# Optimization experiments

Measured on AMD Instinct MI355X. Metric: run time of the kernel, lower is better.

Reference implementation:

```python
import jax, jax.numpy as jnp
import numpy as np

N_NODES = 20000
N_EDGES = 320000
IN_DIM = 128
HID = 64
LATENT = 32
NUM_GRAPHS = 64
NEG_SLOPE = 0.2
BN_EPS = 1e-5


def setup_inputs() -> dict:
    key = jax.random.key(0)
    ks = jax.random.split(key, 24)
    def glorot(k, shape):
        fan_in, fan_out = shape[0], shape[-1]
        lim = (6.0 / (fan_in + fan_out)) ** 0.5
        return jax.random.uniform(k, shape, jnp.float32, -lim, lim)
    inp = {
        "x": jax.random.normal(ks[0], (N_NODES, IN_DIM), jnp.float32),
        "edge_index": jax.random.randint(ks[1], (2, N_EDGES), 0, N_NODES, jnp.int64),
        "batch": jnp.sort(jax.random.randint(ks[2], (N_NODES,), 0, NUM_GRAPHS, jnp.int64)),
        # layer 0: in=128 -> out=64, heads=4
        "Wl0": glorot(ks[3], (IN_DIM, 4 * HID)),
        "Wr0": glorot(ks[4], (IN_DIM, 4 * HID)),
        "att0": glorot(ks[5], (4, HID)),
        "b0": jnp.zeros((4 * HID,), jnp.float32),
        # layer 1: in=256 -> out=64, heads=4
        "Wl1": glorot(ks[6], (4 * HID, 4 * HID)),
        "Wr1": glorot(ks[7], (4 * HID, 4 * HID)),
        "att1": glorot(ks[8], (4, HID)),
        "b1": jnp.zeros((4 * HID,), jnp.float32),
        # layer 2: in=256 -> out=64, heads=1
        "Wl2": glorot(ks[9], (4 * HID, HID)),
        "Wr2": glorot(ks[10], (4 * HID, HID)),
        "att2": glorot(ks[11], (1, HID)),
        "b2": jnp.zeros((HID,), jnp.float32),
        # BatchNorm1d(hidden_dim) in eval mode (running stats)
        "bn_gamma": jax.random.uniform(ks[12], (HID,), jnp.float32, 0.5, 1.5),
        "bn_beta": jax.random.normal(ks[13], (HID,), jnp.float32) * 0.1,
        "bn_mean": jax.random.normal(ks[14], (HID,), jnp.float32) * 0.1,
        "bn_var": jax.random.uniform(ks[15], (HID,), jnp.float32, 0.5, 1.5),
        # fc: hidden -> latent
        "fc_w": glorot(ks[16], (HID, LATENT)),
        "fc_b": jnp.zeros((LATENT,), jnp.float32),
    }
    return inp


def gatv2_layer(h, src, dst, Wl, Wr, att, bias):
    # PyG GATv2Conv (concat=True, negative_slope=0.2, self loops already in src/dst)
    N = h.shape[0]
    H, C = att.shape
    xl = (h @ Wl).reshape(N, H, C)  # source transform
    xr = (h @ Wr).reshape(N, H, C)  # target transform
    e = jax.nn.leaky_relu(xl[src] + xr[dst], NEG_SLOPE)   # [E,H,C]
    logits = jnp.einsum("ehc,hc->eh", e, att)             # [E,H]
    # softmax over incoming edges per destination node
    m = jax.ops.segment_max(logits, dst, num_segments=N)  # [N,H]
    ex = jnp.exp(logits - m[dst])
    denom = jax.ops.segment_sum(ex, dst, num_segments=N)
    alpha = ex / denom[dst]                               # [E,H]
    out = jax.ops.segment_sum(alpha[:, :, None] * xl[src], dst, num_segments=N)
    return out.reshape(N, H * C) + bias


def reference(x, edge_index, batch, Wl0, Wr0, att0, b0, Wl1, Wr1, att1, b1,
              Wl2, Wr2, att2, b2, bn_gamma, bn_beta, bn_mean, bn_var, fc_w, fc_b):
    N = x.shape[0]
    loop = jnp.arange(N, dtype=edge_index.dtype)
    src = jnp.concatenate([edge_index[0], loop])  # add self loops (PyG default)
    dst = jnp.concatenate([edge_index[1], loop])
    h = gatv2_layer(x, src, dst, Wl0, Wr0, att0, b0)   # dropout: eval mode -> identity
    h = gatv2_layer(h, src, dst, Wl1, Wr1, att1, b1)
    h = gatv2_layer(h, src, dst, Wl2, Wr2, att2, b2)   # [N, HID]
    pooled = jax.ops.segment_sum(h, batch, num_segments=NUM_GRAPHS)  # global_add_pool
    bn = (pooled - bn_mean) * jax.lax.rsqrt(bn_var + BN_EPS) * bn_gamma + bn_beta
    return bn @ fc_w + fc_b  # [NUM_GRAPHS, LATENT]
```

## Files before the change

### kernel.cpp

```cpp
#include <hip/hip_runtime.h>
#include <math.h>

#define N_NODES 20000
#define E_ORIG  320000
#define E_TOT   340000
#define NUM_GRAPHS 64
#define SLOTS 96

typedef __attribute__((ext_vector_type(8))) short bf16x8;
typedef __attribute__((ext_vector_type(4))) float f32x4;

__device__ __forceinline__ ushort f2bf(float x) {
  unsigned u = __float_as_uint(x);
  return (ushort)((u + 0x7fffu + ((u >> 16) & 1u)) >> 16);
}
__device__ __forceinline__ float4 ld_bf16x4(const ushort* p) {
  ushort4 u = *(const ushort4*)p;
  float4 f;
  f.x = __uint_as_float((unsigned)u.x << 16);
  f.y = __uint_as_float((unsigned)u.y << 16);
  f.z = __uint_as_float((unsigned)u.z << 16);
  f.w = __uint_as_float((unsigned)u.w << 16);
  return f;
}
__device__ __forceinline__ void gl_lds16(const void* g, void* l) {
  __builtin_amdgcn_global_load_lds(
      (const __attribute__((address_space(1))) unsigned*)(uintptr_t)g,
      (__attribute__((address_space(3))) unsigned*)(uintptr_t)l, 16, 0, 0);
}

__global__ __launch_bounds__(256) void prep(
    const float* __restrict__ x,
    const float* __restrict__ Wl0, const float* __restrict__ Wr0,
    const float* __restrict__ Wl1, const float* __restrict__ Wr1,
    const float* __restrict__ Wl2, const float* __restrict__ Wr2,
    ushort* __restrict__ x16, ushort* __restrict__ Bt0,
    ushort* __restrict__ Bt1, ushort* __restrict__ Bt2,
    int* __restrict__ cursor)
{
  const int Z0 = 640000;
  const int Z1 = Z0 + 65536;
  const int Z2 = Z1 + 131072;
  const int Z3 = Z2 + 32768;
  const int Z4 = Z3 + N_NODES / 4;
  int t = blockIdx.x * 256 + threadIdx.x;
  if (t < Z0) {
    int i = t << 2;
    float4 v = *(const float4*)&x[i];
    ushort4 o; o.x = f2bf(v.x); o.y = f2bf(v.y); o.z = f2bf(v.z); o.w = f2bf(v.w);
    *(ushort4*)&x16[i] = o;
  } else if (t < Z1) {
    int idx = t - Z0; int n = idx >> 7, k = idx & 127;
    float v = (n < 256) ? Wl0[k * 256 + n] : Wr0[k * 256 + (n - 256)];
    Bt0[idx] = f2bf(v);
  } else if (t < Z2) {
    int idx = t - Z1; int n = idx >> 8, k = idx & 255;
    float v = (n < 256) ? Wl1[k * 256 + n] : Wr1[k * 256 + (n - 256)];
    Bt1[idx] = f2bf(v);
  } else if (t < Z3) {
    int idx = t - Z2; int n = idx >> 8, k = idx & 255;
    float v = (n < 64) ? Wl2[k * 64 + n] : Wr2[k * 64 + (n - 64)];
    Bt2[idx] = f2bf(v);
  } else if (t < Z4) {
    int4 z = {0, 0, 0, 0};
    *(int4*)&cursor[(t - Z3) << 2] = z;
  }
}

__device__ __forceinline__ void gemm_body(
    const ushort* __restrict__ A, const ushort* __restrict__ Bt,
    ushort* __restrict__ C, int M, int K, int N, int bid, int tid, char* smem)
{
  ushort* As = (ushort*)smem;
  ushort* Bs = As + 8192;

  const int mtiles = (M + 127) >> 7;
  const int xcd = bid & 7;
  const int i = bid >> 3;
  const int n0 = (i / 20) << 7;
  const int m = xcd + ((i % 20) << 3);
  if (m >= mtiles) return;
  const int m0 = m << 7;

  const int lane = tid & 63;
  const int w = tid >> 6;
  const int wm = (w >> 1) << 6;
  const int wn = (w & 1) << 6;
  const int quad = lane >> 4;
  const int l15 = lane & 15;

  f32x4 acc[4][4] = {};

  for (int k0 = 0; k0 < K; k0 += 64) {
    #pragma unroll
    for (int r = 0; r < 4; r++) {
      int c = (r << 8) + tid;
      int row = c >> 3;
      int col = (c & 7) << 3;
      int ga = m0 + row; if (ga >= M) ga = M - 1;
      gl_lds16(A  + (size_t)ga * K + k0 + col, (char*)As + c * 16);
      gl_lds16(Bt + (size_t)(n0 + row) * K + k0 + col, (char*)Bs + c * 16);
    }
    __syncthreads();
    #pragma unroll
    for (int ks = 0; ks < 2; ks++) {
      bf16x8 af[4], bfr[4];
      #pragma unroll
      for (int ii = 0; ii < 4; ii++)
        af[ii]  = *(const bf16x8*)&As[(wm + (ii << 4) + l15) * 64 + (ks << 5) + (quad << 3)];
      #pragma unroll
      for (int j = 0; j < 4; j++)
        bfr[j] = *(const bf16x8*)&Bs[(wn + (j << 4) + l15) * 64 + (ks << 5) + (quad << 3)];
      #pragma unroll
      for (int ii = 0; ii < 4; ii++)
        #pragma unroll
        for (int j = 0; j < 4; j++)
          acc[ii][j] = __builtin_amdgcn_mfma_f32_16x16x32_bf16(
              af[ii], bfr[j], acc[ii][j], 0, 0, 0);
    }
    __syncthreads();
  }

  ushort* Cs = (ushort*)smem + w * 4608;
  #pragma unroll
  for (int ii = 0; ii < 4; ii++)
    #pragma unroll
    for (int j = 0; j < 4; j++)
      #pragma unroll
      for (int r = 0; r < 4; r++)
        Cs[((ii << 4) + (quad << 2) + r) * 72 + (j << 4) + l15] = f2bf(acc[ii][j][r]);
  #pragma unroll
  for (int it = 0; it < 8; it++) {
    int row = (it << 3) + (lane >> 3);
    int cc = lane & 7;
    bf16x8 v = *(const bf16x8*)&Cs[row * 72 + (cc << 3)];
    int grow = m0 + wm + row;
    if (grow < M)
      *(bf16x8*)&C[(size_t)grow * N + n0 + wn + (cc << 3)] = v;
  }
}

__global__ __launch_bounds__(256) void mfma_gemm_bf16(
    const ushort* __restrict__ A, const ushort* __restrict__ Bt,
    ushort* __restrict__ C, int M, int K, int N)
{
  __shared__ char smem[36864];
  gemm_body(A, Bt, C, M, K, N, blockIdx.x, threadIdx.x, smem);
}

#define FILLB 1329
__global__ __launch_bounds__(256) void gemm0_fill(
    const ushort* __restrict__ x16, const ushort* __restrict__ Bt0,
    ushort* __restrict__ Cbig,
    const int* __restrict__ esrc, const int* __restrict__ edst,
    int* __restrict__ cursor, int* __restrict__ csr_src)
{
  __shared__ char smem[36864];
  const int bid = blockIdx.x;
  if (bid < FILLB) {
    int e = bid * 256 + threadIdx.x;
    if (e >= E_TOT) return;
    int src, dst;
    if (e < E_ORIG) { src = esrc[e]; dst = edst[e]; }
    else            { src = dst = e - E_ORIG; }
    int pos = atomicAdd(&cursor[dst], 1);
    if (pos < SLOTS) csr_src[(size_t)dst * SLOTS + pos] = src;
    return;
  }
  gemm_body(x16, Bt0, Cbig, N_NODES, 128, 512, bid - FILLB, threadIdx.x, smem);
}

__device__ __forceinline__ void h4_term(
    float4 xlv, const float4& xrv, const float4& attv, float& v)
{
  float4 a;
  a.x = xlv.x + xrv.x; a.y = xlv.y + xrv.y;
  a.z = xlv.z + xrv.z; a.w = xlv.w + xrv.w;
  a.x = fmaxf(a.x, 0.2f * a.x); a.y = fmaxf(a.y, 0.2f * a.y);
  a.z = fmaxf(a.z, 0.2f * a.z); a.w = fmaxf(a.w, 0.2f * a.w);
  v = a.x * attv.x + a.y * attv.y + a.z * attv.z + a.w * attv.w;
}

__device__ __forceinline__ void h4_edge(
    const float4& xv, const float4& xrv, const float4& attv,
    float4& acc, float& lsum)
{
  float v;
  h4_term(xv, xrv, attv, v);
  v += __shfl_xor(v, 1);
  v += __shfl_xor(v, 2);
  v += __shfl_xor(v, 4);
  v += __shfl_xor(v, 8);
  float w = __expf(v);
  lsum += w;
  acc.x += w * xv.x; acc.y += w * xv.y;
  acc.z += w * xv.z; acc.w += w * xv.w;
}

__global__ __launch_bounds__(256) void gat_gather_h4(
    const ushort* __restrict__ Cin, const float* __restrict__ att,
    const float* __restrict__ bias, const int* __restrict__ cnt,
    const int* __restrict__ csr_src, ushort* __restrict__ hout)
{
  const int n = blockIdx.x * 4 + (threadIdx.x >> 6);
  const int lane = threadIdx.x & 63;
  const int c4 = lane << 2;
  const float4 xrv  = ld_bf16x4(Cin + (size_t)n * 512 + 256 + c4);
  const float4 attv = *(const float4*)&att[c4];
  const int beg = n * SLOTS;
  int deg = cnt[n]; if (deg > SLOTS) deg = SLOTS;
  const int end = beg + deg;
  float4 acc = make_float4(0.f, 0.f, 0.f, 0.f);
  float lsum = 0.f;
  int p = beg;
  for (; p + 7 < end; p += 8) {
    int s0 = csr_src[p],     s1 = csr_src[p + 1];
    int s2 = csr_src[p + 2], s3 = csr_src[p + 3];
    int s4 = csr_src[p + 4], s5 = csr_src[p + 5];
    int s6 = csr_src[p + 6], s7 = csr_src[p + 7];
    float4 x0 = ld_bf16x4(Cin + (size_t)s0 * 512 + c4);
    float4 x1 = ld_bf16x4(Cin + (size_t)s1 * 512 + c4);
    float4 x2 = ld_bf16x4(Cin + (size_t)s2 * 512 + c4);
    float4 x3 = ld_bf16x4(Cin + (size_t)s3 * 512 + c4);
    float4 x4 = ld_bf16x4(Cin + (size_t)s4 * 512 + c4);
    float4 x5 = ld_bf16x4(Cin + (size_t)s5 * 512 + c4);
    float4 x6 = ld_bf16x4(Cin + (size_t)s6 * 512 + c4);
    float4 x7 = ld_bf16x4(Cin + (size_t)s7 * 512 + c4);
    h4_edge(x0, xrv, attv, acc, lsum);
    h4_edge(x1, xrv, attv, acc, lsum);
    h4_edge(x2, xrv, attv, acc, lsum);
    h4_edge(x3, xrv, attv, acc, lsum);
    h4_edge(x4, xrv, attv, acc, lsum);
    h4_edge(x5, xrv, attv, acc, lsum);
    h4_edge(x6, xrv, attv, acc, lsum);
    h4_edge(x7, xrv, attv, acc, lsum);
  }
  for (; p + 3 < end; p += 4) {
    int s0 = csr_src[p],     s1 = csr_src[p + 1];
    int s2 = csr_src[p + 2], s3 = csr_src[p + 3];
    float4 x0 = ld_bf16x4(Cin + (size_t)s0 * 512 + c4);
    float4 x1 = ld_bf16x4(Cin + (size_t)s1 * 512 + c4);
    float4 x2 = ld_bf16x4(Cin + (size_t)s2 * 512 + c4);
    float4 x3 = ld_bf16x4(Cin + (size_t)s3 * 512 + c4);
    h4_edge(x0, xrv, attv, acc, lsum);
    h4_edge(x1, xrv, attv, acc, lsum);
    h4_edge(x2, xrv, attv, acc, lsum);
    h4_edge(x3, xrv, attv, acc, lsum);
  }
  for (; p < end; p++) {
    int s0 = csr_src[p];
    float4 x0 = ld_bf16x4(Cin + (size_t)s0 * 512 + c4);
    h4_edge(x0, xrv, attv, acc, lsum);
  }
  const float4 bv = *(const float4*)&bias[c4];
  float inv = 1.f / lsum;
  ushort4 o;
  o.x = f2bf(acc.x * inv + bv.x); o.y = f2bf(acc.y * inv + bv.y);
  o.z = f2bf(acc.z * inv + bv.z); o.w = f2bf(acc.w * inv + bv.w);
  *(ushort4*)&hout[(size_t)n * 256 + c4] = o;
}

__global__ __launch_bounds__(256) void gat_gather_h1(
    const ushort* __restrict__ Cin, const float* __restrict__ att,
    const float* __restrict__ bias, const int* __restrict__ cnt,
    const int* __restrict__ csr_src, float* __restrict__ h3)
{
  const int n = blockIdx.x * 4 + (threadIdx.x >> 6);
  const int lane = threadIdx.x & 63;
  const int g = lane >> 4, c4 = (lane & 15) << 2;
  const float4 xrv  = ld_bf16x4(Cin + (size_t)n * 128 + 64 + c4);
  const float4 attv = *(const float4*)&att[c4];
  const int beg = n * SLOTS;
  int deg = cnt[n]; if (deg > SLOTS) deg = SLOTS;
  const int end = beg + deg;
  float4 acc = make_float4(0.f, 0.f, 0.f, 0.f);
  float lsum = 0.f;
  int p = beg + g;
  for (; p + 4 < end; p += 8) {
    int s0 = csr_src[p], s1 = csr_src[p + 4];
    float4 x0 = ld_bf16x4(Cin + (size_t)s0 * 128 + c4);
    float4 x1 = ld_bf16x4(Cin + (size_t)s1 * 128 + c4);
    h4_edge(x0, xrv, attv, acc, lsum);
    h4_edge(x1, xrv, attv, acc, lsum);
  }
  if (p < end) {
    int s0 = csr_src[p];
    float4 x0 = ld_bf16x4(Cin + (size_t)s0 * 128 + c4);
    h4_edge(x0, xrv, attv, acc, lsum);
  }
  #pragma unroll
  for (int off = 16; off <= 32; off <<= 1) {
    lsum  += __shfl_xor(lsum, off);
    acc.x += __shfl_xor(acc.x, off); acc.y += __shfl_xor(acc.y, off);
    acc.z += __shfl_xor(acc.z, off); acc.w += __shfl_xor(acc.w, off);
  }
  if (g == 0) {
    const float4 bv = *(const float4*)&bias[c4];
    float inv = 1.f / lsum;
    float4 o;
    o.x = acc.x * inv + bv.x; o.y = acc.y * inv + bv.y;
    o.z = acc.z * inv + bv.z; o.w = acc.w * inv + bv.w;
    *(float4*)&h3[(size_t)n * 64 + c4] = o;
  }
}

__global__ __launch_bounds__(256) void pool_bn_fc(
    const float* __restrict__ h3, const int* __restrict__ batch,
    const float* __restrict__ gamma, const float* __restrict__ beta,
    const float* __restrict__ mean, const float* __restrict__ var,
    const float* __restrict__ fcw, const float* __restrict__ fcb,
    float* __restrict__ out)
{
  __shared__ float red[256];
  __shared__ float s[64];
  const int g = blockIdx.x;
  const int t = threadIdx.x;
  const int c = t & 63, r = t >> 6;
  int lo = 0, hi = N_NODES;
  while (lo < hi) { int mid = (lo + hi) >> 1; if (batch[mid] < g) lo = mid + 1; else hi = mid; }
  int s0 = lo;
  hi = N_NODES;
  while (lo < hi) { int mid = (lo + hi) >> 1; if (batch[mid] < g + 1) lo = mid + 1; else hi = mid; }
  int e0 = lo;
  float a = 0.f;
  for (int n = s0 + r; n < e0; n += 4) a += h3[(size_t)n * 64 + c];
  red[t] = a;
  __syncthreads();
  if (r == 0) {
    float p = red[c] + red[c + 64] + red[c + 128] + red[c + 192];
    s[c] = (p - mean[c]) * rsqrtf(var[c] + 1e-5f) * gamma[c] + beta[c];
  }
  __syncthreads();
  if (t < 32) {
    float acc = fcb[t];
    #pragma unroll
    for (int k = 0; k < 64; k++) acc += s[k] * fcw[k * 32 + t];
    out[g * 32 + t] = acc;
  }
}

extern "C" void kernel_launch(void* const* d_in, const int* in_sizes, int n_in,
                              void* d_out, int out_size, void* d_ws, size_t ws_size,
                              hipStream_t stream) {
  const float* x    = (const float*)d_in[0];
  const int*   ei   = (const int*)d_in[1];
  const int*   batch= (const int*)d_in[2];
  const float* Wl0  = (const float*)d_in[3];
  const float* Wr0  = (const float*)d_in[4];
  const float* att0 = (const float*)d_in[5];
  const float* b0   = (const float*)d_in[6];
  const float* Wl1  = (const float*)d_in[7];
  const float* Wr1  = (const float*)d_in[8];
  const float* att1 = (const float*)d_in[9];
  const float* b1   = (const float*)d_in[10];
  const float* Wl2  = (const float*)d_in[11];
  const float* Wr2  = (const float*)d_in[12];
  const float* att2 = (const float*)d_in[13];
  const float* b2   = (const float*)d_in[14];
  const float* bng  = (const float*)d_in[15];
  const float* bnb  = (const float*)d_in[16];
  const float* bnm  = (const float*)d_in[17];
  const float* bnv  = (const float*)d_in[18];
  const float* fcw  = (const float*)d_in[19];
  const float* fcb  = (const float*)d_in[20];
  float* out = (float*)d_out;

  const int* esrc = ei;
  const int* edst = ei + E_ORIG;

  char* w = (char*)d_ws;
  ushort* x16  = (ushort*)w;                 w += (size_t)N_NODES * 128 * 2;
  ushort* Cbig = (ushort*)w;                 w += (size_t)N_NODES * 512 * 2;
  ushort* h16  = (ushort*)w;                 w += (size_t)N_NODES * 256 * 2;
  ushort* C2   = (ushort*)w;                 w += (size_t)N_NODES * 128 * 2;
  float*  h3   = (float*)w;                  w += (size_t)N_NODES * 64 * 4;
  ushort* Bt0  = (ushort*)w;                 w += (size_t)512 * 128 * 2;
  ushort* Bt1  = (ushort*)w;                 w += (size_t)512 * 256 * 2;
  ushort* Bt2  = (ushort*)w;                 w += (size_t)128 * 256 * 2;
  int* cursor  = (int*)w;                    w += (size_t)N_NODES * 4;
  int* csr_src = (int*)w;

  dim3 blk(256);

  prep<<<dim3(3416), blk, 0, stream>>>(
      x, Wl0, Wr0, Wl1, Wr1, Wl2, Wr2, x16, Bt0, Bt1, Bt2, cursor);

  gemm0_fill<<<dim3(FILLB + 160 * 4), blk, 0, stream>>>(
      x16, Bt0, Cbig, esrc, edst, cursor, csr_src);

  gat_gather_h4<<<dim3(N_NODES / 4), blk, 0, stream>>>(
      Cbig, att0, b0, cursor, csr_src, h16);

  mfma_gemm_bf16<<<dim3(160 * 4), blk, 0, stream>>>(h16, Bt1, Cbig, N_NODES, 256, 512);
  gat_gather_h4<<<dim3(N_NODES / 4), blk, 0, stream>>>(
      Cbig, att1, b1, cursor, csr_src, h16);

  mfma_gemm_bf16<<<dim3(160 * 1), blk, 0, stream>>>(h16, Bt2, C2, N_NODES, 256, 128);
  gat_gather_h1<<<dim3(N_NODES / 4), blk, 0, stream>>>(
      C2, att2, b2, cursor, csr_src, h3);

  pool_bn_fc<<<dim3(NUM_GRAPHS), blk, 0, stream>>>(
      h3, batch, bng, bnb, bnm, bnv, fcw, fcb, out);
}
```

Before: 261.1 us.

## Fuse all stages into one persistent cooperative kernel with grid syncs

Replaces the eight separate launches (prep, fill plus GEMM0, three gathers, two GEMMs, pool) with one cooperative persistent kernel. Grid-stride loops cover each stage, and a grid.sync separates dependent phases. The aim is to remove per-launch overhead and inter-kernel gaps. In exchange it caps resident blocks per CU through the occupancy query and launch bounds, adds seven grid-wide barriers, and shares one 36 KB shared-memory buffer across phases, which may cost occupancy in the gather phases.

```diff
diff --git a/kernel.cpp b/kernel.cpp
--- a/kernel.cpp
+++ b/kernel.cpp
@@ -1,11 +1,24 @@
 #include <hip/hip_runtime.h>
+#include <hip/hip_cooperative_groups.h>
 #include <math.h>
+
+namespace cg = cooperative_groups;
 
 #define N_NODES 20000
 #define E_ORIG  320000
 #define E_TOT   340000
 #define NUM_GRAPHS 64
 #define SLOTS 96
+#define FILLB 1329
+#define G0B   640
+#define G1B   640
+#define G2B   160
+
+#define PZ0 640000
+#define PZ1 (PZ0 + 65536)
+#define PZ2 (PZ1 + 131072)
+#define PZ3 (PZ2 + 32768)
+#define PZ4 (PZ3 + N_NODES / 4)
 
 typedef __attribute__((ext_vector_type(8))) short bf16x8;
 typedef __attribute__((ext_vector_type(4))) float f32x4;
@@ -29,43 +42,15 @@
       (__attribute__((address_space(3))) unsigned*)(uintptr_t)l, 16, 0, 0);
 }
 
-__global__ __launch_bounds__(256) void prep(
-    const float* __restrict__ x,
-    const float* __restrict__ Wl0, const float* __restrict__ Wr0,
-    const float* __restrict__ Wl1, const float* __restrict__ Wr1,
-    const float* __restrict__ Wl2, const float* __restrict__ Wr2,
-    ushort* __restrict__ x16, ushort* __restrict__ Bt0,
-    ushort* __restrict__ Bt1, ushort* __restrict__ Bt2,
-    int* __restrict__ cursor)
-{
-  const int Z0 = 640000;
-  const int Z1 = Z0 + 65536;
-  const int Z2 = Z1 + 131072;
-  const int Z3 = Z2 + 32768;
-  const int Z4 = Z3 + N_NODES / 4;
-  int t = blockIdx.x * 256 + threadIdx.x;
-  if (t < Z0) {
-    int i = t << 2;
-    float4 v = *(const float4*)&x[i];
-    ushort4 o; o.x = f2bf(v.x); o.y = f2bf(v.y); o.z = f2bf(v.z); o.w = f2bf(v.w);
-    *(ushort4*)&x16[i] = o;
-  } else if (t < Z1) {
-    int idx = t - Z0; int n = idx >> 7, k = idx & 127;
-    float v = (n < 256) ? Wl0[k * 256 + n] : Wr0[k * 256 + (n - 256)];
-    Bt0[idx] = f2bf(v);
-  } else if (t < Z2) {
-    int idx = t - Z1; int n = idx >> 8, k = idx & 255;
-    float v = (n < 256) ? Wl1[k * 256 + n] : Wr1[k * 256 + (n - 256)];
-    Bt1[idx] = f2bf(v);
-  } else if (t < Z3) {
-    int idx = t - Z2; int n = idx >> 8, k = idx & 255;
-    float v = (n < 64) ? Wl2[k * 64 + n] : Wr2[k * 64 + (n - 64)];
-    Bt2[idx] = f2bf(v);
-  } else if (t < Z4) {
-    int4 z = {0, 0, 0, 0};
-    *(int4*)&cursor[(t - Z3) << 2] = z;
-  }
-}
+struct Params {
+  const float* x; const int* esrc; const int* edst; const int* batch;
+  const float *Wl0, *Wr0, *Wl1, *Wr1, *Wl2, *Wr2;
+  const float *att0, *b0, *att1, *b1, *att2, *b2;
+  const float *bng, *bnb, *bnm, *bnv, *fcw, *fcb;
+  float* out;
+  ushort *x16, *Cbig, *h16, *C2; float* h3;
+  ushort *Bt0, *Bt1, *Bt2; int* cursor; int* csr;
+};
 
 __device__ __forceinline__ void gemm_body(
     const ushort* __restrict__ A, const ushort* __restrict__ Bt,
@@ -140,53 +125,16 @@
   }
 }
 
-__global__ __launch_bounds__(256) void mfma_gemm_bf16(
-    const ushort* __restrict__ A, const ushort* __restrict__ Bt,
-    ushort* __restrict__ C, int M, int K, int N)
-{
-  __shared__ char smem[36864];
-  gemm_body(A, Bt, C, M, K, N, blockIdx.x, threadIdx.x, smem);
-}
-
-#define FILLB 1329
-__global__ __launch_bounds__(256) void gemm0_fill(
-    const ushort* __restrict__ x16, const ushort* __restrict__ Bt0,
-    ushort* __restrict__ Cbig,
-    const int* __restrict__ esrc, const int* __restrict__ edst,
-    int* __restrict__ cursor, int* __restrict__ csr_src)
-{
-  __shared__ char smem[36864];
-  const int bid = blockIdx.x;
-  if (bid < FILLB) {
-    int e = bid * 256 + threadIdx.x;
-    if (e >= E_TOT) return;
-    int src, dst;
-    if (e < E_ORIG) { src = esrc[e]; dst = edst[e]; }
-    else            { src = dst = e - E_ORIG; }
-    int pos = atomicAdd(&cursor[dst], 1);
-    if (pos < SLOTS) csr_src[(size_t)dst * SLOTS + pos] = src;
-    return;
-  }
-  gemm_body(x16, Bt0, Cbig, N_NODES, 128, 512, bid - FILLB, threadIdx.x, smem);
-}
-
-__device__ __forceinline__ void h4_term(
-    float4 xlv, const float4& xrv, const float4& attv, float& v)
-{
-  float4 a;
-  a.x = xlv.x + xrv.x; a.y = xlv.y + xrv.y;
-  a.z = xlv.z + xrv.z; a.w = xlv.w + xrv.w;
-  a.x = fmaxf(a.x, 0.2f * a.x); a.y = fmaxf(a.y, 0.2f * a.y);
-  a.z = fmaxf(a.z, 0.2f * a.z); a.w = fmaxf(a.w, 0.2f * a.w);
-  v = a.x * attv.x + a.y * attv.y + a.z * attv.z + a.w * attv.w;
-}
-
 __device__ __forceinline__ void h4_edge(
     const float4& xv, const float4& xrv, const float4& attv,
     float4& acc, float& lsum)
 {
-  float v;
-  h4_term(xv, xrv, attv, v);
+  float4 a;
+  a.x = xv.x + xrv.x; a.y = xv.y + xrv.y;
+  a.z = xv.z + xrv.z; a.w = xv.w + xrv.w;
+  a.x = fmaxf(a.x, 0.2f * a.x); a.y = fmaxf(a.y, 0.2f * a.y);
+  a.z = fmaxf(a.z, 0.2f * a.z); a.w = fmaxf(a.w, 0.2f * a.w);
+  float v = a.x * attv.x + a.y * attv.y + a.z * attv.z + a.w * attv.w;
   v += __shfl_xor(v, 1);
   v += __shfl_xor(v, 2);
   v += __shfl_xor(v, 4);
@@ -197,13 +145,11 @@
   acc.z += w * xv.z; acc.w += w * xv.w;
 }
 
-__global__ __launch_bounds__(256) void gat_gather_h4(
+__device__ __forceinline__ void gat_h4_node(
     const ushort* __restrict__ Cin, const float* __restrict__ att,
     const float* __restrict__ bias, const int* __restrict__ cnt,
-    const int* __restrict__ csr_src, ushort* __restrict__ hout)
-{
-  const int n = blockIdx.x * 4 + (threadIdx.x >> 6);
-  const int lane = threadIdx.x & 63;
+    const int* __restrict__ csr, ushort* __restrict__ hout, int n, int lane)
+{
   const int c4 = lane << 2;
   const float4 xrv  = ld_bf16x4(Cin + (size_t)n * 512 + 256 + c4);
   const float4 attv = *(const float4*)&att[c4];
@@ -214,10 +160,10 @@
   float lsum = 0.f;
   int p = beg;
   for (; p + 7 < end; p += 8) {
-    int s0 = csr_src[p],     s1 = csr_src[p + 1];
-    int s2 = csr_src[p + 2], s3 = csr_src[p + 3];
-    int s4 = csr_src[p + 4], s5 = csr_src[p + 5];
-    int s6 = csr_src[p + 6], s7 = csr_src[p + 7];
+    int s0 = csr[p],     s1 = csr[p + 1];
+    int s2 = csr[p + 2], s3 = csr[p + 3];
+    int s4 = csr[p + 4], s5 = csr[p + 5];
+    int s6 = csr[p + 6], s7 = csr[p + 7];
     float4 x0 = ld_bf16x4(Cin + (size_t)s0 * 512 + c4);
     float4 x1 = ld_bf16x4(Cin + (size_t)s1 * 512 + c4);
     float4 x2 = ld_bf16x4(Cin + (size_t)s2 * 512 + c4);
@@ -236,8 +182,8 @@
     h4_edge(x7, xrv, attv, acc, lsum);
   }
   for (; p + 3 < end; p += 4) {
-    int s0 = csr_src[p],     s1 = csr_src[p + 1];
-    int s2 = csr_src[p + 2], s3 = csr_src[p + 3];
+    int s0 = csr[p],     s1 = csr[p + 1];
+    int s2 = csr[p + 2], s3 = csr[p + 3];
     float4 x0 = ld_bf16x4(Cin + (size_t)s0 * 512 + c4);
     float4 x1 = ld_bf16x4(Cin + (size_t)s1 * 512 + c4);
     float4 x2 = ld_bf16x4(Cin + (size_t)s2 * 512 + c4);
@@ -248,7 +194,7 @@
     h4_edge(x3, xrv, attv, acc, lsum);
   }
   for (; p < end; p++) {
-    int s0 = csr_src[p];
+    int s0 = csr[p];
     float4 x0 = ld_bf16x4(Cin + (size_t)s0 * 512 + c4);
     h4_edge(x0, xrv, attv, acc, lsum);
   }
@@ -260,13 +206,11 @@
   *(ushort4*)&hout[(size_t)n * 256 + c4] = o;
 }
 
-__global__ __launch_bounds__(256) void gat_gather_h1(
+__device__ __forceinline__ void gat_h1_node(
     const ushort* __restrict__ Cin, const float* __restrict__ att,
     const float* __restrict__ bias, const int* __restrict__ cnt,
-    const int* __restrict__ csr_src, float* __restrict__ h3)
-{
-  const int n = blockIdx.x * 4 + (threadIdx.x >> 6);
-  const int lane = threadIdx.x & 63;
+    const int* __restrict__ csr, float* __restrict__ h3, int n, int lane)
+{
   const int g = lane >> 4, c4 = (lane & 15) << 2;
   const float4 xrv  = ld_bf16x4(Cin + (size_t)n * 128 + 64 + c4);
   const float4 attv = *(const float4*)&att[c4];
@@ -277,14 +221,14 @@
   float lsum = 0.f;
   int p = beg + g;
   for (; p + 4 < end; p += 8) {
-    int s0 = csr_src[p], s1 = csr_src[p + 4];
+    int s0 = csr[p], s1 = csr[p + 4];
     float4 x0 = ld_bf16x4(Cin + (size_t)s0 * 128 + c4);
     float4 x1 = ld_bf16x4(Cin + (size_t)s1 * 128 + c4);
     h4_edge(x0, xrv, attv, acc, lsum);
     h4_edge(x1, xrv, attv, acc, lsum);
   }
   if (p < end) {
-    int s0 = csr_src[p];
+    int s0 = csr[p];
     float4 x0 = ld_bf16x4(Cin + (size_t)s0 * 128 + c4);
     h4_edge(x0, xrv, attv, acc, lsum);
   }
@@ -304,101 +248,156 @@
   }
 }
 
-__global__ __launch_bounds__(256) void pool_bn_fc(
-    const float* __restrict__ h3, const int* __restrict__ batch,
-    const float* __restrict__ gamma, const float* __restrict__ beta,
-    const float* __restrict__ mean, const float* __restrict__ var,
-    const float* __restrict__ fcw, const float* __restrict__ fcb,
-    float* __restrict__ out)
-{
-  __shared__ float red[256];
-  __shared__ float s[64];
-  const int g = blockIdx.x;
-  const int t = threadIdx.x;
+__device__ __forceinline__ void pool_body(const Params& p, int g, int t, float* sm)
+{
+  float* red = sm;
+  float* s   = sm + 256;
   const int c = t & 63, r = t >> 6;
   int lo = 0, hi = N_NODES;
-  while (lo < hi) { int mid = (lo + hi) >> 1; if (batch[mid] < g) lo = mid + 1; else hi = mid; }
+  while (lo < hi) { int mid = (lo + hi) >> 1; if (p.batch[mid] < g) lo = mid + 1; else hi = mid; }
   int s0 = lo;
   hi = N_NODES;
-  while (lo < hi) { int mid = (lo + hi) >> 1; if (batch[mid] < g + 1) lo = mid + 1; else hi = mid; }
+  while (lo < hi) { int mid = (lo + hi) >> 1; if (p.batch[mid] < g + 1) lo = mid + 1; else hi = mid; }
   int e0 = lo;
   float a = 0.f;
-  for (int n = s0 + r; n < e0; n += 4) a += h3[(size_t)n * 64 + c];
+  for (int n = s0 + r; n < e0; n += 4) a += p.h3[(size_t)n * 64 + c];
   red[t] = a;
   __syncthreads();
   if (r == 0) {
-    float p = red[c] + red[c + 64] + red[c + 128] + red[c + 192];
-    s[c] = (p - mean[c]) * rsqrtf(var[c] + 1e-5f) * gamma[c] + beta[c];
+    float q = red[c] + red[c + 64] + red[c + 128] + red[c + 192];
+    s[c] = (q - p.bnm[c]) * rsqrtf(p.bnv[c] + 1e-5f) * p.bng[c] + p.bnb[c];
   }
   __syncthreads();
   if (t < 32) {
-    float acc = fcb[t];
+    float acc = p.fcb[t];
     #pragma unroll
-    for (int k = 0; k < 64; k++) acc += s[k] * fcw[k * 32 + t];
-    out[g * 32 + t] = acc;
-  }
+    for (int k = 0; k < 64; k++) acc += s[k] * p.fcw[k * 32 + t];
+    p.out[g * 32 + t] = acc;
+  }
+  __syncthreads();
+}
+
+__global__ __launch_bounds__(256, 3) void fused_all(Params p)
+{
+  __shared__ char smem[36864];
+  const int bid = blockIdx.x, tid = threadIdx.x;
+  const int NB = gridDim.x;
+  const int lane = tid & 63, wv = tid >> 6;
+  cg::grid_group grid = cg::this_grid();
+
+  for (int t = bid * 256 + tid; t < PZ4; t += NB * 256) {
+    if (t < PZ0) {
+      int i = t << 2;
+      float4 v = *(const float4*)&p.x[i];
+      ushort4 o; o.x = f2bf(v.x); o.y = f2bf(v.y); o.z = f2bf(v.z); o.w = f2bf(v.w);
+      *(ushort4*)&p.x16[i] = o;
+    } else if (t < PZ1) {
+      int idx = t - PZ0; int n = idx >> 7, k = idx & 127;
+      float v = (n < 256) ? p.Wl0[k * 256 + n] : p.Wr0[k * 256 + (n - 256)];
+      p.Bt0[idx] = f2bf(v);
+    } else if (t < PZ2) {
+      int idx = t - PZ1; int n = idx >> 8, k = idx & 255;
+      float v = (n < 256) ? p.Wl1[k * 256 + n] : p.Wr1[k * 256 + (n - 256)];
+      p.Bt1[idx] = f2bf(v);
+    } else if (t < PZ3) {
+      int idx = t - PZ2; int n = idx >> 8, k = idx & 255;
+      float v = (n < 64) ? p.Wl2[k * 64 + n] : p.Wr2[k * 64 + (n - 64)];
+      p.Bt2[idx] = f2bf(v);
+    } else {
+      int4 z = {0, 0, 0, 0};
+      *(int4*)&p.cursor[(t - PZ3) << 2] = z;
+    }
+  }
+  grid.sync();
+
+  for (int r = bid; r < FILLB + G0B; r += NB) {
+    if (r < FILLB) {
+      int e = r * 256 + tid;
+      if (e < E_TOT) {
+        int src, dst;
+        if (e < E_ORIG) { src = p.esrc[e]; dst = p.edst[e]; }
+        else            { src = dst = e - E_ORIG; }
+        int pos = atomicAdd(&p.cursor[dst], 1);
+        if (pos < SLOTS) p.csr[(size_t)dst * SLOTS + pos] = src;
+      }
+    } else {
+      gemm_body(p.x16, p.Bt0, p.Cbig, N_NODES, 128, 512, r - FILLB, tid, smem);
+    }
+  }
+  grid.sync();
+
+  for (int b = bid; b < N_NODES / 4; b += NB)
+    gat_h4_node(p.Cbig, p.att0, p.b0, p.cursor, p.csr, p.h16, b * 4 + wv, lane);
+  grid.sync();
+
+  for (int r = bid; r < G1B; r += NB)
+    gemm_body(p.h16, p.Bt1, p.Cbig, N_NODES, 256, 512, r, tid, smem);
+  grid.sync();
+
+  for (int b = bid; b < N_NODES / 4; b += NB)
+    gat_h4_node(p.Cbig, p.att1, p.b1, p.cursor, p.csr, p.h16, b * 4 + wv, lane);
+  grid.sync();
+
+  for (int r = bid; r < G2B; r += NB)
+    gemm_body(p.h16, p.Bt2, p.C2, N_NODES, 256, 128, r, tid, smem);
+  grid.sync();
+
+  for (int b = bid; b < N_NODES / 4; b += NB)
+    gat_h1_node(p.C2, p.att2, p.b2, p.cursor, p.csr, p.h3, b * 4 + wv, lane);
+  grid.sync();
+
+  for (int g = bid; g < NUM_GRAPHS; g += NB)
+    pool_body(p, g, tid, (float*)smem);
 }
 
 extern "C" void kernel_launch(void* const* d_in, const int* in_sizes, int n_in,
                               void* d_out, int out_size, void* d_ws, size_t ws_size,
                               hipStream_t stream) {
-  const float* x    = (const float*)d_in[0];
-  const int*   ei   = (const int*)d_in[1];
-  const int*   batch= (const int*)d_in[2];
-  const float* Wl0  = (const float*)d_in[3];
-  const float* Wr0  = (const float*)d_in[4];
-  const float* att0 = (const float*)d_in[5];
-  const float* b0   = (const float*)d_in[6];
-  const float* Wl1  = (const float*)d_in[7];
-  const float* Wr1  = (const float*)d_in[8];
-  const float* att1 = (const float*)d_in[9];
-  const float* b1   = (const float*)d_in[10];
-  const float* Wl2  = (const float*)d_in[11];
-  const float* Wr2  = (const float*)d_in[12];
-  const float* att2 = (const float*)d_in[13];
-  const float* b2   = (const float*)d_in[14];
-  const float* bng  = (const float*)d_in[15];
-  const float* bnb  = (const float*)d_in[16];
-  const float* bnm  = (const float*)d_in[17];
-  const float* bnv  = (const float*)d_in[18];
-  const float* fcw  = (const float*)d_in[19];
-  const float* fcb  = (const float*)d_in[20];
-  float* out = (float*)d_out;
-
-  const int* esrc = ei;
-  const int* edst = ei + E_ORIG;
+  const int* ei = (const int*)d_in[1];
+
+  Params p;
+  p.x    = (const float*)d_in[0];
+  p.esrc = ei;
+  p.edst = ei + E_ORIG;
+  p.batch= (const int*)d_in[2];
+  p.Wl0  = (const float*)d_in[3];
+  p.Wr0  = (const float*)d_in[4];
+  p.att0 = (const float*)d_in[5];
+  p.b0   = (const float*)d_in[6];
+  p.Wl1  = (const float*)d_in[7];
+  p.Wr1  = (const float*)d_in[8];
+  p.att1 = (const float*)d_in[9];
+  p.b1   = (const float*)d_in[10];
+  p.Wl2  = (const float*)d_in[11];
+  p.Wr2  = (const float*)d_in[12];
+  p.att2 = (const float*)d_in[13];
+  p.b2   = (const float*)d_in[14];
+  p.bng  = (const float*)d_in[15];
+  p.bnb  = (const float*)d_in[16];
+  p.bnm  = (const float*)d_in[17];
+  p.bnv  = (const float*)d_in[18];
+  p.fcw  = (const float*)d_in[19];
+  p.fcb  = (const float*)d_in[20];
+  p.out  = (float*)d_out;
 
   char* w = (char*)d_ws;
-  ushort* x16  = (ushort*)w;                 w += (size_t)N_NODES * 128 * 2;
-  ushort* Cbig = (ushort*)w;                 w += (size_t)N_NODES * 512 * 2;
-  ushort* h16  = (ushort*)w;                 w += (size_t)N_NODES * 256 * 2;
-  ushort* C2   = (ushort*)w;                 w += (size_t)N_NODES * 128 * 2;
-  float*  h3   = (float*)w;                  w += (size_t)N_NODES * 64 * 4;
-  ushort* Bt0  = (ushort*)w;                 w += (size_t)512 * 128 * 2;
-  ushort* Bt1  = (ushort*)w;                 w += (size_t)512 * 256 * 2;
-  ushort* Bt2  = (ushort*)w;                 w += (size_t)128 * 256 * 2;
-  int* cursor  = (int*)w;                    w += (size_t)N_NODES * 4;
-  int* csr_src = (int*)w;
-
-  dim3 blk(256);
-
-  prep<<<dim3(3416), blk, 0, stream>>>(
-      x, Wl0, Wr0, Wl1, Wr1, Wl2, Wr2, x16, Bt0, Bt1, Bt2, cursor);
-
-  gemm0_fill<<<dim3(FILLB + 160 * 4), blk, 0, stream>>>(
-      x16, Bt0, Cbig, esrc, edst, cursor, csr_src);
-
-  gat_gather_h4<<<dim3(N_NODES / 4), blk, 0, stream>>>(
-      Cbig, att0, b0, cursor, csr_src, h16);
-
-  mfma_gemm_bf16<<<dim3(160 * 4), blk, 0, stream>>>(h16, Bt1, Cbig, N_NODES, 256, 512);
-  gat_gather_h4<<<dim3(N_NODES / 4), blk, 0, stream>>>(
-      Cbig, att1, b1, cursor, csr_src, h16);
-
-  mfma_gemm_bf16<<<dim3(160 * 1), blk, 0, stream>>>(h16, Bt2, C2, N_NODES, 256, 128);
-  gat_gather_h1<<<dim3(N_NODES / 4), blk, 0, stream>>>(
-      C2, att2, b2, cursor, csr_src, h3);
-
-  pool_bn_fc<<<dim3(NUM_GRAPHS), blk, 0, stream>>>(
-      h3, batch, bng, bnb, bnm, bnv, fcw, fcb, out);
-}
+  p.x16  = (ushort*)w;                 w += (size_t)N_NODES * 128 * 2;
+  p.Cbig = (ushort*)w;                 w += (size_t)N_NODES * 512 * 2;
+  p.h16  = (ushort*)w;                 w += (size_t)N_NODES * 256 * 2;
+  p.C2   = (ushort*)w;                 w += (size_t)N_NODES * 128 * 2;
+  p.h3   = (float*)w;                  w += (size_t)N_NODES * 64 * 4;
+  p.Bt0  = (ushort*)w;                 w += (size_t)512 * 128 * 2;
+  p.Bt1  = (ushort*)w;                 w += (size_t)512 * 256 * 2;
+  p.Bt2  = (ushort*)w;                 w += (size_t)128 * 256 * 2;
+  p.cursor = (int*)w;                  w += (size_t)N_NODES * 4;
+  p.csr  = (int*)w;
+
+  int nb = 0;
+  hipOccupancyMaxActiveBlocksPerMultiprocessor(&nb, fused_all, 256, 0);
+  if (nb < 1) nb = 1;
+  if (nb > 4) nb = 4;
+  int grid = nb * 256;
+
+  void* args[] = { (void*)&p };
+  hipLaunchCooperativeKernel(fused_all, dim3(grid), dim3(256), args, 0, stream);
+}
```

Measured after the change: 656.3 us. +151.4%, slower.

## Split XL/XR into separate buffers, handle self-loops inline, shrink CSR slots

Applied to the files above, without the earlier changes.

The GEMM epilogue now writes the source and target projections into two separate contiguous arrays instead of one interleaved 512-wide row, so the gather reads a denser 256-wide XL array with better cache locality. Self-loop edges are no longer inserted through atomics into the CSR; each gather processes the node's own XL row directly. CSR slots shrink from 96 to 64 per node, which reduces the memory footprint but drops edges for any node whose in-degree exceeds 64.

```diff
diff --git a/kernel.cpp b/kernel.cpp
--- a/kernel.cpp
+++ b/kernel.cpp
@@ -3,9 +3,9 @@
 
 #define N_NODES 20000
 #define E_ORIG  320000
-#define E_TOT   340000
 #define NUM_GRAPHS 64
-#define SLOTS 96
+#define SLOTS 64
+#define FILLB 1250
 
 typedef __attribute__((ext_vector_type(8))) short bf16x8;
 typedef __attribute__((ext_vector_type(4))) float f32x4;
@@ -69,7 +69,8 @@
 
 __device__ __forceinline__ void gemm_body(
     const ushort* __restrict__ A, const ushort* __restrict__ Bt,
-    ushort* __restrict__ C, int M, int K, int N, int bid, int tid, char* smem)
+    ushort* __restrict__ XL, ushort* __restrict__ XR,
+    int M, int K, int N, int bid, int tid, char* smem)
 {
   ushort* As = (ushort*)smem;
   ushort* Bs = As + 8192;
@@ -129,6 +130,9 @@
       #pragma unroll
       for (int r = 0; r < 4; r++)
         Cs[((ii << 4) + (quad << 2) + r) * 72 + (j << 4) + l15] = f2bf(acc[ii][j][r]);
+  const int Nh = N >> 1;
+  const int colbase = n0 + wn;
+  ushort* Cc = (colbase < Nh) ? (XL + colbase) : (XR + (colbase - Nh));
   #pragma unroll
   for (int it = 0; it < 8; it++) {
     int row = (it << 3) + (lane >> 3);
@@ -136,22 +140,21 @@
     bf16x8 v = *(const bf16x8*)&Cs[row * 72 + (cc << 3)];
     int grow = m0 + wm + row;
     if (grow < M)
-      *(bf16x8*)&C[(size_t)grow * N + n0 + wn + (cc << 3)] = v;
+      *(bf16x8*)&Cc[(size_t)grow * Nh + (cc << 3)] = v;
   }
 }
 
 __global__ __launch_bounds__(256) void mfma_gemm_bf16(
     const ushort* __restrict__ A, const ushort* __restrict__ Bt,
-    ushort* __restrict__ C, int M, int K, int N)
+    ushort* __restrict__ XL, ushort* __restrict__ XR, int M, int K, int N)
 {
   __shared__ char smem[36864];
-  gemm_body(A, Bt, C, M, K, N, blockIdx.x, threadIdx.x, smem);
-}
-
-#define FILLB 1329
+  gemm_body(A, Bt, XL, XR, M, K, N, blockIdx.x, threadIdx.x, smem);
+}
+
 __global__ __launch_bounds__(256) void gemm0_fill(
     const ushort* __restrict__ x16, const ushort* __restrict__ Bt0,
-    ushort* __restrict__ Cbig,
+    ushort* __restrict__ XL, ushort* __restrict__ XR,
     const int* __restrict__ esrc, const int* __restrict__ edst,
     int* __restrict__ cursor, int* __restrict__ csr_src)
 {
@@ -159,34 +162,25 @@
   const int bid = blockIdx.x;
   if (bid < FILLB) {
     int e = bid * 256 + threadIdx.x;
-    if (e >= E_TOT) return;
-    int src, dst;
-    if (e < E_ORIG) { src = esrc[e]; dst = edst[e]; }
-    else            { src = dst = e - E_ORIG; }
+    if (e >= E_ORIG) return;
+    int src = esrc[e], dst = edst[e];
     int pos = atomicAdd(&cursor[dst], 1);
-    if (pos < SLOTS) csr_src[(size_t)dst * SLOTS + pos] = src;
+    if (pos < SLOTS) csr_src[((size_t)dst << 6) + pos] = src;
     return;
   }
-  gemm_body(x16, Bt0, Cbig, N_NODES, 128, 512, bid - FILLB, threadIdx.x, smem);
-}
-
-__device__ __forceinline__ void h4_term(
-    float4 xlv, const float4& xrv, const float4& attv, float& v)
-{
-  float4 a;
-  a.x = xlv.x + xrv.x; a.y = xlv.y + xrv.y;
-  a.z = xlv.z + xrv.z; a.w = xlv.w + xrv.w;
-  a.x = fmaxf(a.x, 0.2f * a.x); a.y = fmaxf(a.y, 0.2f * a.y);
-  a.z = fmaxf(a.z, 0.2f * a.z); a.w = fmaxf(a.w, 0.2f * a.w);
-  v = a.x * attv.x + a.y * attv.y + a.z * attv.z + a.w * attv.w;
+  gemm_body(x16, Bt0, XL, XR, N_NODES, 128, 512, bid - FILLB, threadIdx.x, smem);
 }
 
 __device__ __forceinline__ void h4_edge(
     const float4& xv, const float4& xrv, const float4& attv,
     float4& acc, float& lsum)
 {
-  float v;
-  h4_term(xv, xrv, attv, v);
+  float4 a;
+  a.x = xv.x + xrv.x; a.y = xv.y + xrv.y;
+  a.z = xv.z + xrv.z; a.w = xv.w + xrv.w;
+  a.x = fmaxf(a.x, 0.2f * a.x); a.y = fmaxf(a.y, 0.2f * a.y);
+  a.z = fmaxf(a.z, 0.2f * a.z); a.w = fmaxf(a.w, 0.2f * a.w);
+  float v = a.x * attv.x + a.y * attv.y + a.z * attv.z + a.w * attv.w;
   v += __shfl_xor(v, 1);
   v += __shfl_xor(v, 2);
   v += __shfl_xor(v, 4);
@@ -198,34 +192,39 @@
 }
 
 __global__ __launch_bounds__(256) void gat_gather_h4(
-    const ushort* __restrict__ Cin, const float* __restrict__ att,
-    const float* __restrict__ bias, const int* __restrict__ cnt,
-    const int* __restrict__ csr_src, ushort* __restrict__ hout)
+    const ushort* __restrict__ XL, const ushort* __restrict__ XR,
+    const float* __restrict__ att, const float* __restrict__ bias,
+    const int* __restrict__ cnt, const int* __restrict__ csr,
+    ushort* __restrict__ hout)
 {
   const int n = blockIdx.x * 4 + (threadIdx.x >> 6);
   const int lane = threadIdx.x & 63;
   const int c4 = lane << 2;
-  const float4 xrv  = ld_bf16x4(Cin + (size_t)n * 512 + 256 + c4);
+  const float4 xrv  = ld_bf16x4(XR + (size_t)n * 256 + c4);
   const float4 attv = *(const float4*)&att[c4];
-  const int beg = n * SLOTS;
+  float4 acc = make_float4(0.f, 0.f, 0.f, 0.f);
+  float lsum = 0.f;
+  {
+    float4 xs = ld_bf16x4(XL + (size_t)n * 256 + c4);
+    h4_edge(xs, xrv, attv, acc, lsum);
+  }
+  const int beg = n << 6;
   int deg = cnt[n]; if (deg > SLOTS) deg = SLOTS;
   const int end = beg + deg;
-  float4 acc = make_float4(0.f, 0.f, 0.f, 0.f);
-  float lsum = 0.f;
   int p = beg;
   for (; p + 7 < end; p += 8) {
-    int s0 = csr_src[p],     s1 = csr_src[p + 1];
-    int s2 = csr_src[p + 2], s3 = csr_src[p + 3];
-    int s4 = csr_src[p + 4], s5 = csr_src[p + 5];
-    int s6 = csr_src[p + 6], s7 = csr_src[p + 7];
-    float4 x0 = ld_bf16x4(Cin + (size_t)s0 * 512 + c4);
-    float4 x1 = ld_bf16x4(Cin + (size_t)s1 * 512 + c4);
-    float4 x2 = ld_bf16x4(Cin + (size_t)s2 * 512 + c4);
-    float4 x3 = ld_bf16x4(Cin + (size_t)s3 * 512 + c4);
-    float4 x4 = ld_bf16x4(Cin + (size_t)s4 * 512 + c4);
-    float4 x5 = ld_bf16x4(Cin + (size_t)s5 * 512 + c4);
-    float4 x6 = ld_bf16x4(Cin + (size_t)s6 * 512 + c4);
-    float4 x7 = ld_bf16x4(Cin + (size_t)s7 * 512 + c4);
+    int s0 = csr[p],     s1 = csr[p + 1];
+    int s2 = csr[p + 2], s3 = csr[p + 3];
+    int s4 = csr[p + 4], s5 = csr[p + 5];
+    int s6 = csr[p + 6], s7 = csr[p + 7];
+    float4 x0 = ld_bf16x4(XL + (size_t)s0 * 256 + c4);
+    float4 x1 = ld_bf16x4(XL + (size_t)s1 * 256 + c4);
+    float4 x2 = ld_bf16x4(XL + (size_t)s2 * 256 + c4);
+    float4 x3 = ld_bf16x4(XL + (size_t)s3 * 256 + c4);
+    float4 x4 = ld_bf16x4(XL + (size_t)s4 * 256 + c4);
+    float4 x5 = ld_bf16x4(XL + (size_t)s5 * 256 + c4);
+    float4 x6 = ld_bf16x4(XL + (size_t)s6 * 256 + c4);
+    float4 x7 = ld_bf16x4(XL + (size_t)s7 * 256 + c4);
     h4_edge(x0, xrv, attv, acc, lsum);
     h4_edge(x1, xrv, attv, acc, lsum);
     h4_edge(x2, xrv, attv, acc, lsum);
@@ -236,20 +235,20 @@
     h4_edge(x7, xrv, attv, acc, lsum);
   }
   for (; p + 3 < end; p += 4) {
-    int s0 = csr_src[p],     s1 = csr_src[p + 1];
-    int s2 = csr_src[p + 2], s3 = csr_src[p + 3];
-    float4 x0 = ld_bf16x4(Cin + (size_t)s0 * 512 + c4);
-    float4 x1 = ld_bf16x4(Cin + (size_t)s1 * 512 + c4);
-    float4 x2 = ld_bf16x4(Cin + (size_t)s2 * 512 + c4);
-    float4 x3 = ld_bf16x4(Cin + (size_t)s3 * 512 + c4);
+    int s0 = csr[p],     s1 = csr[p + 1];
+    int s2 = csr[p + 2], s3 = csr[p + 3];
+    float4 x0 = ld_bf16x4(XL + (size_t)s0 * 256 + c4);
+    float4 x1 = ld_bf16x4(XL + (size_t)s1 * 256 + c4);
+    float4 x2 = ld_bf16x4(XL + (size_t)s2 * 256 + c4);
+    float4 x3 = ld_bf16x4(XL + (size_t)s3 * 256 + c4);
     h4_edge(x0, xrv, attv, acc, lsum);
     h4_edge(x1, xrv, attv, acc, lsum);
     h4_edge(x2, xrv, attv, acc, lsum);
     h4_edge(x3, xrv, attv, acc, lsum);
   }
   for (; p < end; p++) {
-    int s0 = csr_src[p];
-    float4 x0 = ld_bf16x4(Cin + (size_t)s0 * 512 + c4);
+    int s0 = csr[p];
+    float4 x0 = ld_bf16x4(XL + (size_t)s0 * 256 + c4);
     h4_edge(x0, xrv, attv, acc, lsum);
   }
   const float4 bv = *(const float4*)&bias[c4];
@@ -261,31 +260,36 @@
 }
 
 __global__ __launch_bounds__(256) void gat_gather_h1(
-    const ushort* __restrict__ Cin, const float* __restrict__ att,
-    const float* __restrict__ bias, const int* __restrict__ cnt,
-    const int* __restrict__ csr_src, float* __restrict__ h3)
+    const ushort* __restrict__ XL, const ushort* __restrict__ XR,
+    const float* __restrict__ att, const float* __restrict__ bias,
+    const int* __restrict__ cnt, const int* __restrict__ csr,
+    float* __restrict__ h3)
 {
   const int n = blockIdx.x * 4 + (threadIdx.x >> 6);
   const int lane = threadIdx.x & 63;
   const int g = lane >> 4, c4 = (lane & 15) << 2;
-  const float4 xrv  = ld_bf16x4(Cin + (size_t)n * 128 + 64 + c4);
+  const float4 xrv  = ld_bf16x4(XR + (size_t)n * 64 + c4);
   const float4 attv = *(const float4*)&att[c4];
-  const int beg = n * SLOTS;
+  float4 acc = make_float4(0.f, 0.f, 0.f, 0.f);
+  float lsum = 0.f;
+  if (g == 0) {
+    float4 xs = ld_bf16x4(XL + (size_t)n * 64 + c4);
+    h4_edge(xs, xrv, attv, acc, lsum);
+  }
+  const int beg = n << 6;
   int deg = cnt[n]; if (deg > SLOTS) deg = SLOTS;
   const int end = beg + deg;
-  float4 acc = make_float4(0.f, 0.f, 0.f, 0.f);
-  float lsum = 0.f;
   int p = beg + g;
   for (; p + 4 < end; p += 8) {
-    int s0 = csr_src[p], s1 = csr_src[p + 4];
-    float4 x0 = ld_bf16x4(Cin + (size_t)s0 * 128 + c4);
-    float4 x1 = ld_bf16x4(Cin + (size_t)s1 * 128 + c4);
+    int s0 = csr[p], s1 = csr[p + 4];
+    float4 x0 = ld_bf16x4(XL + (size_t)s0 * 64 + c4);
+    float4 x1 = ld_bf16x4(XL + (size_t)s1 * 64 + c4);
     h4_edge(x0, xrv, attv, acc, lsum);
     h4_edge(x1, xrv, attv, acc, lsum);
   }
   if (p < end) {
-    int s0 = csr_src[p];
-    float4 x0 = ld_bf16x4(Cin + (size_t)s0 * 128 + c4);
+    int s0 = csr[p];
+    float4 x0 = ld_bf16x4(XL + (size_t)s0 * 64 + c4);
     h4_edge(x0, xrv, attv, acc, lsum);
   }
   #pragma unroll
@@ -370,15 +374,17 @@
 
   char* w = (char*)d_ws;
   ushort* x16  = (ushort*)w;                 w += (size_t)N_NODES * 128 * 2;
-  ushort* Cbig = (ushort*)w;                 w += (size_t)N_NODES * 512 * 2;
+  ushort* XL   = (ushort*)w;                 w += (size_t)N_NODES * 256 * 2;
+  ushort* XR   = (ushort*)w;                 w += (size_t)N_NODES * 256 * 2;
   ushort* h16  = (ushort*)w;                 w += (size_t)N_NODES * 256 * 2;
-  ushort* C2   = (ushort*)w;                 w += (size_t)N_NODES * 128 * 2;
+  ushort* XL2  = (ushort*)w;                 w += (size_t)N_NODES * 64 * 2;
+  ushort* XR2  = (ushort*)w;                 w += (size_t)N_NODES * 64 * 2;
   float*  h3   = (float*)w;                  w += (size_t)N_NODES * 64 * 4;
   ushort* Bt0  = (ushort*)w;                 w += (size_t)512 * 128 * 2;
   ushort* Bt1  = (ushort*)w;                 w += (size_t)512 * 256 * 2;
   ushort* Bt2  = (ushort*)w;                 w += (size_t)128 * 256 * 2;
   int* cursor  = (int*)w;                    w += (size_t)N_NODES * 4;
-  int* csr_src = (int*)w;
+  int* csr     = (int*)w;
 
   dim3 blk(256);
 
@@ -386,18 +392,18 @@
       x, Wl0, Wr0, Wl1, Wr1, Wl2, Wr2, x16, Bt0, Bt1, Bt2, cursor);
 
   gemm0_fill<<<dim3(FILLB + 160 * 4), blk, 0, stream>>>(
-      x16, Bt0, Cbig, esrc, edst, cursor, csr_src);
+      x16, Bt0, XL, XR, esrc, edst, cursor, csr);
 
   gat_gather_h4<<<dim3(N_NODES / 4), blk, 0, stream>>>(
-      Cbig, att0, b0, cursor, csr_src, h16);
-
-  mfma_gemm_bf16<<<dim3(160 * 4), blk, 0, stream>>>(h16, Bt1, Cbig, N_NODES, 256, 512);
+      XL, XR, att0, b0, cursor, csr, h16);
+
+  mfma_gemm_bf16<<<dim3(160 * 4), blk, 0, stream>>>(h16, Bt1, XL, XR, N_NODES, 256, 512);
   gat_gather_h4<<<dim3(N_NODES / 4), blk, 0, stream>>>(
-      Cbig, att1, b1, cursor, csr_src, h16);
-
-  mfma_gemm_bf16<<<dim3(160 * 1), blk, 0, stream>>>(h16, Bt2, C2, N_NODES, 256, 128);
+      XL, XR, att1, b1, cursor, csr, h16);
+
+  mfma_gemm_bf16<<<dim3(160 * 1), blk, 0, stream>>>(h16, Bt2, XL2, XR2, N_NODES, 256, 128);
   gat_gather_h1<<<dim3(N_NODES / 4), blk, 0, stream>>>(
-      C2, att2, b2, cursor, csr_src, h3);
+      XL2, XR2, att2, b2, cursor, csr, h3);
 
   pool_bn_fc<<<dim3(NUM_GRAPHS), blk, 0, stream>>>(
       h3, batch, bng, bnb, bnm, bnv, fcw, fcb, out);
```

New measurement: 262.4 us, median of 2. Within noise of the previous version (+0.5%).
